# Optimization experiments

Measured on AMD Instinct MI355X. Metric: run time of the kernel, lower is better.

Reference implementation:

```python
import jax, jax.numpy as jnp
import numpy as np

DIM = 1024
HEADS = 16
HEAD_DIM = DIM // HEADS
RANK = 4
AUDIO_DIM = 768


def _lora(x, A, B):
    # x: [..., in]; A: [rank, in]; B: [out, rank]
    return x + (x @ A.T @ B.T) * (1.0 / RANK)


def setup_inputs() -> dict:
    key = jax.random.key(0)
    ks = jax.random.split(key, 20)
    s = 0.02
    inp = {
        "x": jax.random.normal(ks[0], (1, 4096, DIM), jnp.float32),
        "audio_features": jax.random.normal(ks[1], (1, 1024, AUDIO_DIM), jnp.float32),
        "q_w": jax.random.normal(ks[2], (DIM, DIM), jnp.float32) * s,
        "q_b": jnp.zeros((DIM,), jnp.float32),
        "k_w": jax.random.normal(ks[3], (DIM, DIM), jnp.float32) * s,
        "k_b": jnp.zeros((DIM,), jnp.float32),
        "v_w": jax.random.normal(ks[4], (DIM, DIM), jnp.float32) * s,
        "v_b": jnp.zeros((DIM,), jnp.float32),
        "o_w": jax.random.normal(ks[5], (DIM, DIM), jnp.float32) * s,
        "o_b": jnp.zeros((DIM,), jnp.float32),
        "a_w": jax.random.normal(ks[6], (DIM, AUDIO_DIM), jnp.float32) * s,
        "a_b": jnp.zeros((DIM,), jnp.float32),
        "qA": jax.random.normal(ks[7], (RANK, DIM), jnp.float32) * 0.01,
        "qB": jax.random.normal(ks[8], (DIM, RANK), jnp.float32) * 0.01,
        "kA": jax.random.normal(ks[9], (RANK, DIM), jnp.float32) * 0.01,
        "kB": jax.random.normal(ks[10], (DIM, RANK), jnp.float32) * 0.01,
        "vA": jax.random.normal(ks[11], (RANK, DIM), jnp.float32) * 0.01,
        "vB": jax.random.normal(ks[12], (DIM, RANK), jnp.float32) * 0.01,
    }
    return inp


def reference(x, audio_features, q_w, q_b, k_w, k_b, v_w, v_b, o_w, o_b,
              a_w, a_b, qA, qB, kA, kB, vA, vB):
    B, N, C = x.shape
    # audio projection: Linear(768 -> dim), torch Linear is x @ W.T + b
    audio = audio_features @ a_w.T + a_b  # [B, M, C]
    M = audio.shape[1]

    q = _lora(x @ q_w.T + q_b, qA, qB)      # [B, N, C]
    k = _lora(audio @ k_w.T + k_b, kA, kB)  # [B, M, C]
    v = _lora(audio @ v_w.T + v_b, vA, vB)  # [B, M, C]

    q = q.reshape(B, N, HEADS, HEAD_DIM).transpose(0, 2, 1, 3)  # [B,H,N,d]
    k = k.reshape(B, M, HEADS, HEAD_DIM).transpose(0, 2, 1, 3)  # [B,H,M,d]
    v = v.reshape(B, M, HEADS, HEAD_DIM).transpose(0, 2, 1, 3)  # [B,H,M,d]

    scale = HEAD_DIM ** -0.5
    attn = jnp.einsum('bhnd,bhmd->bhnm', q, k) * scale  # [B,H,N,M]
    attn = jax.nn.softmax(attn, axis=-1)
    out = jnp.einsum('bhnm,bhmd->bhnd', attn, v)        # [B,H,N,d]
    out = out.transpose(0, 2, 1, 3).reshape(B, N, C)
    return out @ o_w.T + o_b
```

## Files before the change

### kernel.cpp

```cpp
#include <hip/hip_runtime.h>
#include <math.h>

#define DIM 1024
#define HEADS 16
#define HD 64
#define QSCALE 0.1803368801111204f

typedef __attribute__((ext_vector_type(8))) short short8;
typedef __attribute__((ext_vector_type(4))) float f32x4;
typedef unsigned short ushort_t;

#define MFMA(a, b, c) __builtin_amdgcn_mfma_f32_16x16x32_bf16(a, b, c, 0, 0, 0)
#define VMCNT(n) asm volatile("s_waitcnt vmcnt(" #n ")" ::: "memory")
#define BARRIER() __builtin_amdgcn_s_barrier()

__device__ __forceinline__ ushort_t f2bf(float f) {
    union { float f; unsigned u; } v; v.f = f;
    unsigned r = v.u + 0x7FFF + ((v.u >> 16) & 1);
    return (ushort_t)(r >> 16);
}
__device__ __forceinline__ void gl2lds16(const void* g, void* l) {
    __builtin_amdgcn_global_load_lds(
        (const __attribute__((address_space(1))) unsigned*)g,
        (__attribute__((address_space(3))) unsigned*)l, 16, 0, 0);
}

#define C_X  1048576
#define C_AF 196608
__global__ __launch_bounds__(256) void prep1(
    const float* __restrict__ x, const float* __restrict__ af,
    const float* __restrict__ aw, const float* __restrict__ ow,
    ushort_t* __restrict__ xb, ushort_t* __restrict__ afb,
    ushort_t* __restrict__ awb, ushort_t* __restrict__ owb,
    const float* __restrict__ qw, const float* __restrict__ kw,
    const float* __restrict__ vw,
    const float* __restrict__ qA, const float* __restrict__ kA,
    const float* __restrict__ vA,
    float* __restrict__ part)
{
    const int b = blockIdx.x, tid = threadIdx.x;
    if (b < 6656) {
        int c = b * 256 + tid;
        const float* s; ushort_t* d; int off;
        if (c < C_X)               { s = x;  d = xb;  off = c; }
        else if (c < C_X + C_AF)   { s = af; d = afb; off = c - C_X; }
        else if (c < C_X + 2*C_AF) { s = aw; d = awb; off = c - C_X - C_AF; }
        else                       { s = ow; d = owb; off = c - C_X - 2*C_AF; }
        float4 v = ((const float4*)s)[off];
        ushort4 o = { f2bf(v.x), f2bf(v.y), f2bf(v.z), f2bf(v.w) };
        ((ushort4*)d)[off] = o;
        return;
    }
    const int pb = b - 6656;
    const int proj = pb >> 4, chunk = pb & 15;
    const float* W = proj == 0 ? qw : proj == 1 ? kw : vw;
    const float* A = proj == 0 ? qA : proj == 1 ? kA : vA;
    const float4* W4 = (const float4*)W;

    float4 acc0 = {0,0,0,0}, acc1 = {0,0,0,0}, acc2 = {0,0,0,0}, acc3 = {0,0,0,0};
    const int o0 = chunk * 64;
    for (int o = o0; o < o0 + 64; ++o) {
        float4 wrow = W4[o * 256 + tid];
        float a0 = A[o], a1 = A[1024 + o], a2 = A[2048 + o], a3 = A[3072 + o];
        acc0.x += a0 * wrow.x; acc0.y += a0 * wrow.y; acc0.z += a0 * wrow.z; acc0.w += a0 * wrow.w;
        acc1.x += a1 * wrow.x; acc1.y += a1 * wrow.y; acc1.z += a1 * wrow.z; acc1.w += a1 * wrow.w;
        acc2.x += a2 * wrow.x; acc2.y += a2 * wrow.y; acc2.z += a2 * wrow.z; acc2.w += a2 * wrow.w;
        acc3.x += a3 * wrow.x; acc3.y += a3 * wrow.y; acc3.z += a3 * wrow.z; acc3.w += a3 * wrow.w;
    }
    float4* P4 = (float4*)part;
    P4[(pb * 4 + 0) * 256 + tid] = acc0;
    P4[(pb * 4 + 1) * 256 + tid] = acc1;
    P4[(pb * 4 + 2) * 256 + tid] = acc2;
    P4[(pb * 4 + 3) * 256 + tid] = acc3;
}

__global__ __launch_bounds__(256) void prep2(
    const float* __restrict__ qw, const float* __restrict__ kw,
    const float* __restrict__ vw,
    const float* __restrict__ qA, const float* __restrict__ kA,
    const float* __restrict__ vA,
    const float* __restrict__ qB, const float* __restrict__ kB,
    const float* __restrict__ vB,
    const float* __restrict__ qb, const float* __restrict__ kb,
    const float* __restrict__ vb,
    const float* __restrict__ part,
    ushort_t* __restrict__ wqe, ushort_t* __restrict__ wke,
    ushort_t* __restrict__ wve, float* __restrict__ beff)
{
    const int b = blockIdx.x, tid = threadIdx.x;
    const int proj = b >> 4, chunk = b & 15;
    const float* W = proj == 0 ? qw : proj == 1 ? kw : vw;
    const float* A = proj == 0 ? qA : proj == 1 ? kA : vA;
    const float* B = proj == 0 ? qB : proj == 1 ? kB : vB;
    const float* bias = proj == 0 ? qb : proj == 1 ? kb : vb;
    ushort_t* Weff = proj == 0 ? wqe : proj == 1 ? wke : wve;
    const float scale = proj == 0 ? QSCALE : 1.0f;
    const float4* W4 = (const float4*)W;
    const float4* P4 = (const float4*)part;

    __shared__ float T1s[4096];
    #pragma unroll
    for (int r = 0; r < 4; ++r) {
        float4 s = {0, 0, 0, 0};
        for (int blk = 0; blk < 16; ++blk) {
            float4 p = P4[((proj * 16 + blk) * 4 + r) * 256 + tid];
            s.x += p.x; s.y += p.y; s.z += p.z; s.w += p.w;
        }
        *(float4*)(T1s + r * 1024 + tid * 4) = s;
    }
    __syncthreads();

    float4 t0 = *(const float4*)(T1s + tid * 4);
    float4 t1 = *(const float4*)(T1s + 1024 + tid * 4);
    float4 t2 = *(const float4*)(T1s + 2048 + tid * 4);
    float4 t3 = *(const float4*)(T1s + 3072 + tid * 4);

    const int o0 = chunk * 64;
    for (int o = o0; o < o0 + 64; ++o) {
        float4 wrow = W4[o * 256 + tid];
        float4 Bo = *(const float4*)(B + o * 4);
        ushort4 out;
        out.x = f2bf((wrow.x + 0.25f * (Bo.x*t0.x + Bo.y*t1.x + Bo.z*t2.x + Bo.w*t3.x)) * scale);
        out.y = f2bf((wrow.y + 0.25f * (Bo.x*t0.y + Bo.y*t1.y + Bo.z*t2.y + Bo.w*t3.y)) * scale);
        out.z = f2bf((wrow.z + 0.25f * (Bo.x*t0.z + Bo.y*t1.z + Bo.z*t2.z + Bo.w*t3.z)) * scale);
        out.w = f2bf((wrow.w + 0.25f * (Bo.x*t0.w + Bo.y*t1.w + Bo.z*t2.w + Bo.w*t3.w)) * scale);
        *(ushort4*)(Weff + (size_t)o * 1024 + tid * 4) = out;
    }

    if (chunk == 0) {
        float bt[4] = {0.f, 0.f, 0.f, 0.f};
        for (int o = tid; o < 1024; o += 256) {
            float bo = bias[o];
            bt[0] = fmaf(A[o], bo, bt[0]);
            bt[1] = fmaf(A[1024 + o], bo, bt[1]);
            bt[2] = fmaf(A[2048 + o], bo, bt[2]);
            bt[3] = fmaf(A[3072 + o], bo, bt[3]);
        }
        #pragma unroll
        for (int r = 0; r < 4; ++r)
            #pragma unroll
            for (int off = 32; off; off >>= 1) bt[r] += __shfl_xor(bt[r], off);
        __shared__ float btr[4][4];
        if ((tid & 63) == 0) {
            #pragma unroll
            for (int r = 0; r < 4; ++r) btr[r][tid >> 6] = bt[r];
        }
        __syncthreads();
        float b0 = btr[0][0] + btr[0][1] + btr[0][2] + btr[0][3];
        float b1 = btr[1][0] + btr[1][1] + btr[1][2] + btr[1][3];
        float b2 = btr[2][0] + btr[2][1] + btr[2][2] + btr[2][3];
        float b3 = btr[3][0] + btr[3][1] + btr[3][2] + btr[3][3];
        for (int o = tid; o < 1024; o += 256) {
            float4 Bo = *(const float4*)(B + o * 4);
            beff[proj * 1024 + o] =
                (bias[o] + 0.25f * (Bo.x*b0 + Bo.y*b1 + Bo.z*b2 + Bo.w*b3)) * scale;
        }
    }
}

template<int OUTF32>
__device__ __forceinline__ void gemm3p_body(
    char* lds, const ushort_t* __restrict__ A, const ushort_t* __restrict__ W,
    const float* __restrict__ bias, void* __restrict__ C,
    int N, int K, int bm, int bn)
{
    const int tid = threadIdx.x, lane = tid & 63, wv = tid >> 6;
    const int l15 = lane & 15, l4 = lane >> 4;
    const int wm = wv >> 1, wn = wv & 1;

    const ushort_t *Ag[2], *Wg[2];
    #pragma unroll
    for (int c = 0; c < 2; ++c) {
        int f = c * 256 + tid, ra = f >> 2, ga = (f & 3) ^ ((ra >> 1) & 3);
        Ag[c] = A + (size_t)(bm * 128 + ra) * K + ga * 8;
        Wg[c] = W + (size_t)(bn * 128 + ra) * K + ga * 8;
    }
    int aoff[4], woff[4];
    #pragma unroll
    for (int m = 0; m < 4; ++m) {
        int r = wm * 64 + m * 16 + l15;
        aoff[m] = r * 64 + ((l4 ^ ((r >> 1) & 3)) << 4);
    }
    #pragma unroll
    for (int n = 0; n < 4; ++n) {
        int cc = wn * 64 + n * 16 + l15;
        woff[n] = cc * 64 + ((l4 ^ ((cc >> 1) & 3)) << 4);
    }

    auto stage = [&](char* base, int k0) {
        #pragma unroll
        for (int c = 0; c < 2; ++c) {
            gl2lds16(Ag[c] + k0, base + c * 4096 + wv * 1024);
            gl2lds16(Wg[c] + k0, base + 8192 + c * 4096 + wv * 1024);
        }
    };

    short8 fa[4], fw[4];
    auto readfr = [&](const char* base) {
        #pragma unroll
        for (int m = 0; m < 4; ++m) fa[m] = *(const short8*)(base + aoff[m]);
        #pragma unroll
        for (int n = 0; n < 4; ++n) fw[n] = *(const short8*)(base + 8192 + woff[n]);
    };

    f32x4 acc[4][4] = {};
    const int nt = K / 32;

    stage(lds, 0);
    stage(lds + 16384, 32);
    VMCNT(4);
    BARRIER();
    readfr(lds);

    int bcur = 0;
    for (int t = 0; t < nt; ++t) {
        int bnext = bcur + 1; if (bnext == 3) bnext = 0;
        int bpre  = bnext + 1; if (bpre == 3) bpre = 0;
        if (t + 2 < nt) stage(lds + bpre * 16384, (t + 2) * 32);
        #pragma unroll
        for (int m = 0; m < 4; ++m)
            #pragma unroll
            for (int n = 0; n < 4; ++n)
                acc[m][n] = MFMA(fa[m], fw[n], acc[m][n]);
        if (t + 1 < nt) {
            if (t + 2 < nt) { VMCNT(4); } else { VMCNT(0); }
            BARRIER();
            readfr(lds + bnext * 16384);
        }
        bcur = bnext;
    }

    #pragma unroll
    for (int n = 0; n < 4; ++n) {
        int gc = bn * 128 + wn * 64 + n * 16 + l15;
        float bv = bias[gc];
        #pragma unroll
        for (int m = 0; m < 4; ++m) {
            int gr = bm * 128 + wm * 64 + m * 16 + (l4 << 2);
            #pragma unroll
            for (int j = 0; j < 4; ++j) {
                float v = acc[m][n][j] + bv;
                if (OUTF32) ((float*)C)[(size_t)(gr + j) * N + gc] = v;
                else        ((ushort_t*)C)[(size_t)(gr + j) * N + gc] = f2bf(v);
            }
        }
    }
}

template<int OUTF32>
__global__ __launch_bounds__(256) void gemm3p(
    const ushort_t* __restrict__ A, const ushort_t* __restrict__ W,
    const float* __restrict__ bias, void* __restrict__ C, int N, int K)
{
    __shared__ char lds[49152];
    gemm3p_body<OUTF32>(lds, A, W, bias, C, N, K, blockIdx.y, blockIdx.x);
}

__device__ __forceinline__ void audio_body(
    char* lds, const ushort_t* __restrict__ A, const ushort_t* __restrict__ W,
    const float* __restrict__ bias, ushort_t* __restrict__ C, int bm, int bn)
{
    const int K = 768, N = DIM;
    char* As = lds;
    char* Ws = lds + 8192;
    const int tid = threadIdx.x, lane = tid & 63, wv = tid >> 6;
    const int l15 = lane & 15, l4 = lane >> 4;

    int f = tid, ra = f >> 2, ga = (f & 3) ^ ((ra >> 1) & 3);
    const ushort_t* Ag = A + (size_t)(bm * 64 + ra) * K + ga * 8;
    const ushort_t* Wg = W + (size_t)(bn * 64 + ra) * K + ga * 8;

    int aoff, woff[4];
    { int r = wv * 16 + l15; aoff = r * 64 + ((l4 ^ ((r >> 1) & 3)) << 4); }
    #pragma unroll
    for (int n = 0; n < 4; ++n) {
        int cc = n * 16 + l15;
        woff[n] = cc * 64 + ((l4 ^ ((cc >> 1) & 3)) << 4);
    }

    f32x4 acc[4] = {};
    const int nt = K / 32;
    gl2lds16(Ag, As + wv * 1024);
    gl2lds16(Wg, Ws + wv * 1024);

    for (int t = 0; t < nt; ++t) {
        const int buf = t & 1;
        if (t + 1 < nt) {
            const int k1 = (t + 1) * 32;
            gl2lds16(Ag + k1, As + (buf ^ 1) * 4096 + wv * 1024);
            gl2lds16(Wg + k1, Ws + (buf ^ 1) * 4096 + wv * 1024);
            VMCNT(2);
        } else {
            VMCNT(0);
        }
        BARRIER();
        const char* AsB = As + buf * 4096;
        const char* WsB = Ws + buf * 4096;
        short8 fa = *(const short8*)(AsB + aoff);
        short8 fw[4];
        #pragma unroll
        for (int n = 0; n < 4; ++n) fw[n] = *(const short8*)(WsB + woff[n]);
        #pragma unroll
        for (int n = 0; n < 4; ++n) acc[n] = MFMA(fa, fw[n], acc[n]);
        BARRIER();
    }

    const int gr = bm * 64 + wv * 16 + (l4 << 2);
    #pragma unroll
    for (int n = 0; n < 4; ++n) {
        int gc = bn * 64 + n * 16 + l15;
        float bb = bias[gc];
        #pragma unroll
        for (int j = 0; j < 4; ++j)
            C[(size_t)(gr + j) * N + gc] = f2bf(acc[n][j] + bb);
    }
}

__global__ __launch_bounds__(256) void fused_aq(
    const ushort_t* __restrict__ afb, const ushort_t* __restrict__ awb,
    const float* __restrict__ a_b, ushort_t* __restrict__ audio,
    const ushort_t* __restrict__ xb, const ushort_t* __restrict__ wqe,
    const float* __restrict__ beff, ushort_t* __restrict__ qbb)
{
    __shared__ char lds[49152];
    const int b = blockIdx.x;
    if (b < 256) {
        audio_body(lds, afb, awb, a_b, audio, b >> 4, b & 15);
    } else {
        const int i = b - 256;
        gemm3p_body<0>(lds, xb, wqe, beff, qbb, DIM, DIM, i >> 3, i & 7);
    }
}

__global__ __launch_bounds__(256) void gemm2_kv(
    const ushort_t* __restrict__ A, const ushort_t* __restrict__ Wk,
    const ushort_t* __restrict__ Wv, const float* __restrict__ bk,
    const float* __restrict__ bv, ushort_t* __restrict__ Ck,
    ushort_t* __restrict__ CvT)
{
    const int K = DIM;
    __shared__ ushort_t As[2][64 * 32];
    __shared__ ushort_t Ws[2][64 * 32];
    const int tid = threadIdx.x, lane = tid & 63, wv = tid >> 6;
    const int l15 = lane & 15, l4 = lane >> 4;
    const int bm = blockIdx.y;
    const bool isV = blockIdx.x >= 16;
    const int bn = blockIdx.x & 15;
    const ushort_t* W = isV ? Wv : Wk;

    int f = tid, ra = f >> 2, ga = (f & 3) ^ ((ra >> 1) & 3);
    const ushort_t* Ag = A + (size_t)(bm * 64 + ra) * K + ga * 8;
    const ushort_t* Wg = W + (size_t)(bn * 64 + ra) * K + ga * 8;

    int aoff, woff[4];
    { int r = wv * 16 + l15; aoff = r * 64 + ((l4 ^ ((r >> 1) & 3)) << 4); }
    #pragma unroll
    for (int n = 0; n < 4; ++n) {
        int cc = n * 16 + l15;
        woff[n] = cc * 64 + ((l4 ^ ((cc >> 1) & 3)) << 4);
    }

    f32x4 acc[4] = {};
    const int nt = K / 32;
    gl2lds16(Ag, (char*)As + wv * 1024);
    gl2lds16(Wg, (char*)Ws + wv * 1024);

    for (int t = 0; t < nt; ++t) {
        const int buf = t & 1;
        if (t + 1 < nt) {
            const int k1 = (t + 1) * 32;
            gl2lds16(Ag + k1, (char*)As + (buf ^ 1) * 4096 + wv * 1024);
            gl2lds16(Wg + k1, (char*)Ws + (buf ^ 1) * 4096 + wv * 1024);
            VMCNT(2);
        } else {
            VMCNT(0);
        }
        BARRIER();
        const char* AsB = (const char*)As + buf * 4096;
        const char* WsB = (const char*)Ws + buf * 4096;
        short8 fa = *(const short8*)(AsB + aoff);
        short8 fw[4];
        #pragma unroll
        for (int n = 0; n < 4; ++n) fw[n] = *(const short8*)(WsB + woff[n]);
        #pragma unroll
        for (int n = 0; n < 4; ++n) acc[n] = MFMA(fa, fw[n], acc[n]);
        BARRIER();
    }

    const int gr = bm * 64 + wv * 16 + (l4 << 2);
    #pragma unroll
    for (int n = 0; n < 4; ++n) {
        int gc = bn * 64 + n * 16 + l15;
        float bb = (isV ? bv : bk)[gc];
        if (!isV) {
            #pragma unroll
            for (int j = 0; j < 4; ++j)
                Ck[(size_t)(gr + j) * DIM + gc] = f2bf(acc[n][j] + bb);
        } else {
            ushort4 o = { f2bf(acc[n][0] + bb), f2bf(acc[n][1] + bb),
                          f2bf(acc[n][2] + bb), f2bf(acc[n][3] + bb) };
            *(ushort4*)(CvT + (size_t)gc * DIM + gr) = o;
        }
    }
}

__global__ __launch_bounds__(256) void attn3(
    const ushort_t* __restrict__ Qf, const ushort_t* __restrict__ Kf,
    const ushort_t* __restrict__ Vt, ushort_t* __restrict__ AO)
{
    __shared__ char lds[40960];
    char* QsPs = lds;
    char* KsB0 = lds + 8192;
    char* VsB0 = lds + 24576;

    const int tid = threadIdx.x, lane = tid & 63, wv = tid >> 6;
    const int l15 = lane & 15, l4 = lane >> 4;
    const int h = blockIdx.y, qb = blockIdx.x;

    #pragma unroll
    for (int i = 0; i < 2; ++i) {
        int f = i * 256 + tid, q = f >> 3, s = (f & 7) ^ (q & 7);
        gl2lds16(Qf + (size_t)(qb * 64 + q) * DIM + h * HD + s * 8,
                 QsPs + i * 4096 + wv * 1024);
    }
    const int f0 = tid, r0 = f0 >> 3, s0 = (f0 & 7) ^ (r0 & 7);
    const int f1 = 256 + tid, r1 = f1 >> 3, s1 = (f1 & 7) ^ (r1 & 7);
    const ushort_t* Kg0 = Kf + (size_t)r0 * DIM + h * HD + s0 * 8;
    const ushort_t* Kg1 = Kf + (size_t)r1 * DIM + h * HD + s1 * 8;
    const ushort_t* Vg0 = Vt + (size_t)(h * HD + r0) * DIM + s0 * 8;
    const ushort_t* Vg1 = Vt + (size_t)(h * HD + r1) * DIM + s1 * 8;

    int qoff[2], koff[4][2], poff[2];
    #pragma unroll
    for (int ks = 0; ks < 2; ++ks) {
        int r = wv * 16 + l15;
        qoff[ks] = r * 128 + (((ks * 4 + l4) ^ (r & 7)) << 4);
        poff[ks] = wv * 2048 + l15 * 128 + (((ks * 4 + l4) ^ (l15 & 7)) << 4);
    }
    #pragma unroll
    for (int n = 0; n < 4; ++n) {
        int kk = n * 16 + l15;
        #pragma unroll
        for (int ks = 0; ks < 2; ++ks)
            koff[n][ks] = kk * 128 + (((ks * 4 + l4) ^ (kk & 7)) << 4);
    }

    f32x4 acc_o[4] = {};
    float l_loc[4] = {0.f, 0.f, 0.f, 0.f};

    gl2lds16(Kg0, KsB0 + wv * 1024);
    gl2lds16(Kg1, KsB0 + 4096 + wv * 1024);
    gl2lds16(Vg0, VsB0 + wv * 1024);
    gl2lds16(Vg1, VsB0 + 4096 + wv * 1024);
    VMCNT(4);
    BARRIER();
    short8 fq[2];
    #pragma unroll
    for (int ks = 0; ks < 2; ++ks)
        fq[ks] = *(const short8*)(QsPs + qoff[ks]);

    for (int t = 0; t < 16; ++t) {
        const int buf = t & 1;
        if (t < 15) {
            gl2lds16(Kg0 + (size_t)(t + 1) * 64 * DIM,
                     KsB0 + (buf ^ 1) * 8192 + wv * 1024);
            gl2lds16(Kg1 + (size_t)(t + 1) * 64 * DIM,
                     KsB0 + (buf ^ 1) * 8192 + 4096 + wv * 1024);
            gl2lds16(Vg0 + (t + 1) * 64,
                     VsB0 + (buf ^ 1) * 8192 + wv * 1024);
            gl2lds16(Vg1 + (t + 1) * 64,
                     VsB0 + (buf ^ 1) * 8192 + 4096 + wv * 1024);
            VMCNT(4);
        } else {
            VMCNT(0);
        }
        BARRIER();

        const char* KsT = KsB0 + buf * 8192;
        const char* VsT = VsB0 + buf * 8192;

        f32x4 s_acc[4] = {};
        short8 fk[4][2];
        #pragma unroll
        for (int n = 0; n < 4; ++n)
            #pragma unroll
            for (int ks = 0; ks < 2; ++ks)
                fk[n][ks] = *(const short8*)(KsT + koff[n][ks]);
        #pragma unroll
        for (int n = 0; n < 4; ++n)
            #pragma unroll
            for (int ks = 0; ks < 2; ++ks)
                s_acc[n] = MFMA(fq[ks], fk[n][ks], s_acc[n]);

        #pragma unroll
        for (int j = 0; j < 4; ++j) {
            float p0 = exp2f(s_acc[0][j]);
            float p1 = exp2f(s_acc[1][j]);
            float p2 = exp2f(s_acc[2][j]);
            float p3 = exp2f(s_acc[3][j]);
            l_loc[j] += (p0 + p1) + (p2 + p3);
            unsigned pk01, pk23;
            asm("v_cvt_pk_bf16_f32 %0, %1, %2" : "=v"(pk01) : "v"(p0), "v"(p1));
            asm("v_cvt_pk_bf16_f32 %0, %1, %2" : "=v"(pk23) : "v"(p2), "v"(p3));
            int r16 = (l4 << 2) + j;
            int basb = wv * 2048 + r16 * 128;
            int sw = (r16 & 7) << 4;
            int kx = l15 * 2;
            *(ushort_t*)(QsPs + basb + ((kx) ^ sw))      = (ushort_t)pk01;
            *(ushort_t*)(QsPs + basb + ((32 + kx) ^ sw)) = (ushort_t)(pk01 >> 16);
            *(ushort_t*)(QsPs + basb + ((64 + kx) ^ sw)) = (ushort_t)pk23;
            *(ushort_t*)(QsPs + basb + ((96 + kx) ^ sw)) = (ushort_t)(pk23 >> 16);
        }

        short8 pa[2], fv[4][2];
        #pragma unroll
        for (int ks = 0; ks < 2; ++ks)
            pa[ks] = *(const short8*)(QsPs + poff[ks]);
        #pragma unroll
        for (int n = 0; n < 4; ++n)
            #pragma unroll
            for (int ks = 0; ks < 2; ++ks)
                fv[n][ks] = *(const short8*)(VsT + koff[n][ks]);
        #pragma unroll
        for (int dn = 0; dn < 4; ++dn)
            #pragma unroll
            for (int ks = 0; ks < 2; ++ks)
                acc_o[dn] = MFMA(pa[ks], fv[dn][ks], acc_o[dn]);
        BARRIER();
    }

    #pragma unroll
    for (int j = 0; j < 4; ++j) {
        float l = l_loc[j];
        l += __shfl_xor(l, 1);
        l += __shfl_xor(l, 2);
        l += __shfl_xor(l, 4);
        l += __shfl_xor(l, 8);
        float inv = 1.0f / l;
        int q = qb * 64 + wv * 16 + (l4 << 2) + j;
        #pragma unroll
        for (int dn = 0; dn < 4; ++dn)
            AO[(size_t)q * DIM + h * HD + dn * 16 + l15] =
                f2bf(acc_o[dn][j] * inv);
    }
}

extern "C" void kernel_launch(void* const* d_in, const int* in_sizes, int n_in,
                              void* d_out, int out_size, void* d_ws, size_t ws_size,
                              hipStream_t stream)
{
    const float* x   = (const float*)d_in[0];
    const float* af  = (const float*)d_in[1];
    const float* q_w = (const float*)d_in[2];
    const float* q_b = (const float*)d_in[3];
    const float* k_w = (const float*)d_in[4];
    const float* k_b = (const float*)d_in[5];
    const float* v_w = (const float*)d_in[6];
    const float* v_b = (const float*)d_in[7];
    const float* o_w = (const float*)d_in[8];
    const float* o_b = (const float*)d_in[9];
    const float* a_w = (const float*)d_in[10];
    const float* a_b = (const float*)d_in[11];
    const float* qA  = (const float*)d_in[12];
    const float* qB  = (const float*)d_in[13];
    const float* kA  = (const float*)d_in[14];
    const float* kB  = (const float*)d_in[15];
    const float* vA  = (const float*)d_in[16];
    const float* vB  = (const float*)d_in[17];
    float* out = (float*)d_out;

    const int N = 4096;

    char* w = (char*)d_ws;
    auto alloc = [&](size_t bytes) {
        char* p = w; w += (bytes + 255) & ~(size_t)255; return p;
    };
    ushort_t* xb   = (ushort_t*)alloc((size_t)N * DIM * 2);
    ushort_t* afb  = (ushort_t*)alloc((size_t)1024 * 768 * 2);
    ushort_t* awb  = (ushort_t*)alloc((size_t)DIM * 768 * 2);
    ushort_t* owb  = (ushort_t*)alloc((size_t)DIM * DIM * 2);
    ushort_t* wqe  = (ushort_t*)alloc((size_t)DIM * DIM * 2);
    ushort_t* wke  = (ushort_t*)alloc((size_t)DIM * DIM * 2);
    ushort_t* wve  = (ushort_t*)alloc((size_t)DIM * DIM * 2);
    ushort_t* audio= (ushort_t*)alloc((size_t)1024 * DIM * 2);
    ushort_t* qbb  = (ushort_t*)alloc((size_t)N * DIM * 2);
    ushort_t* kbb  = (ushort_t*)alloc((size_t)1024 * DIM * 2);
    ushort_t* vt   = (ushort_t*)alloc((size_t)1024 * DIM * 2);
    ushort_t* ao   = (ushort_t*)alloc((size_t)N * DIM * 2);
    float* part = (float*)alloc((size_t)48 * 4 * 1024 * 4);
    float* beff = (float*)alloc((size_t)3 * 1024 * 4);

    prep1<<<6704, 256, 0, stream>>>(
        x, af, a_w, o_w, xb, afb, awb, owb,
        q_w, k_w, v_w, qA, kA, vA, part);
    prep2<<<48, 256, 0, stream>>>(
        q_w, k_w, v_w, qA, kA, vA, qB, kB, vB, q_b, k_b, v_b,
        part, wqe, wke, wve, beff);
    fused_aq<<<512, 256, 0, stream>>>(afb, awb, a_b, audio, xb, wqe, beff, qbb);
    gemm2_kv<<<dim3(32, 16), 256, 0, stream>>>(audio, wke, wve,
                                               beff + 1024, beff + 2048, kbb, vt);
    attn3<<<dim3(N / 64, HEADS), 256, 0, stream>>>(qbb, kbb, vt, ao);
    gemm3p<1><<<dim3(8, 32), 256, 0, stream>>>(ao, owb, o_b, out, DIM, DIM);
}
```

Baseline: 230.6 us.

## Split attention keys across two waves with per-wave pipelines and LDS reduction

The attention kernel now runs two waves per block. Each wave owns all 64 queries, holds Q in registers, and processes half of the 1024 keys with its own double-buffered K/V staging, so no block barriers are needed inside the loop. The two partial outputs and row sums are combined through LDS at the end. prep1 also reorders its blocks so the 48 low-rank partial-product blocks are scheduled first. This trades higher register pressure (16 accumulator tiles) and an extra reduction step for fewer barriers and more MFMA work per loaded K/V fragment.

```diff
diff --git a/kernel.cpp b/kernel.cpp
--- a/kernel.cpp
+++ b/kernel.cpp
@@ -12,6 +12,7 @@
 
 #define MFMA(a, b, c) __builtin_amdgcn_mfma_f32_16x16x32_bf16(a, b, c, 0, 0, 0)
 #define VMCNT(n) asm volatile("s_waitcnt vmcnt(" #n ")" ::: "memory")
+#define LGKMCNT0() asm volatile("s_waitcnt lgkmcnt(0)" ::: "memory")
 #define BARRIER() __builtin_amdgcn_s_barrier()
 
 __device__ __forceinline__ ushort_t f2bf(float f) {
@@ -39,8 +40,8 @@
     float* __restrict__ part)
 {
     const int b = blockIdx.x, tid = threadIdx.x;
-    if (b < 6656) {
-        int c = b * 256 + tid;
+    if (b >= 48) {
+        int c = (b - 48) * 256 + tid;
         const float* s; ushort_t* d; int off;
         if (c < C_X)               { s = x;  d = xb;  off = c; }
         else if (c < C_X + C_AF)   { s = af; d = afb; off = c - C_X; }
@@ -51,7 +52,7 @@
         ((ushort4*)d)[off] = o;
         return;
     }
-    const int pb = b - 6656;
+    const int pb = b;
     const int proj = pb >> 4, chunk = pb & 15;
     const float* W = proj == 0 ? qw : proj == 1 ? kw : vw;
     const float* A = proj == 0 ? qA : proj == 1 ? kA : vA;
@@ -404,144 +405,158 @@
     }
 }
 
-__global__ __launch_bounds__(256) void attn3(
+__global__ __launch_bounds__(128) void attn4(
     const ushort_t* __restrict__ Qf, const ushort_t* __restrict__ Kf,
     const ushort_t* __restrict__ Vt, ushort_t* __restrict__ AO)
 {
-    __shared__ char lds[40960];
-    char* QsPs = lds;
-    char* KsB0 = lds + 8192;
-    char* VsB0 = lds + 24576;
-
-    const int tid = threadIdx.x, lane = tid & 63, wv = tid >> 6;
+    __shared__ char lds[41472];
+    char* KL = lds;
+    char* VL = lds + 16384;
+    char* PL = lds + 32768;
+    float* l_arr = (float*)(lds + 40960);
+
+    const int tid = threadIdx.x, lane = tid & 63, w = tid >> 6;
     const int l15 = lane & 15, l4 = lane >> 4;
     const int h = blockIdx.y, qb = blockIdx.x;
-
-    #pragma unroll
-    for (int i = 0; i < 2; ++i) {
-        int f = i * 256 + tid, q = f >> 3, s = (f & 7) ^ (q & 7);
-        gl2lds16(Qf + (size_t)(qb * 64 + q) * DIM + h * HD + s * 8,
-                 QsPs + i * 4096 + wv * 1024);
-    }
-    const int f0 = tid, r0 = f0 >> 3, s0 = (f0 & 7) ^ (r0 & 7);
-    const int f1 = 256 + tid, r1 = f1 >> 3, s1 = (f1 & 7) ^ (r1 & 7);
-    const ushort_t* Kg0 = Kf + (size_t)r0 * DIM + h * HD + s0 * 8;
-    const ushort_t* Kg1 = Kf + (size_t)r1 * DIM + h * HD + s1 * 8;
-    const ushort_t* Vg0 = Vt + (size_t)(h * HD + r0) * DIM + s0 * 8;
-    const ushort_t* Vg1 = Vt + (size_t)(h * HD + r1) * DIM + s1 * 8;
-
-    int qoff[2], koff[4][2], poff[2];
-    #pragma unroll
-    for (int ks = 0; ks < 2; ++ks) {
-        int r = wv * 16 + l15;
-        qoff[ks] = r * 128 + (((ks * 4 + l4) ^ (r & 7)) << 4);
-        poff[ks] = wv * 2048 + l15 * 128 + (((ks * 4 + l4) ^ (l15 & 7)) << 4);
-    }
-    #pragma unroll
-    for (int n = 0; n < 4; ++n) {
+    const int key_base = w * 512;
+
+    short8 fq[4][2];
+    #pragma unroll
+    for (int m = 0; m < 4; ++m)
+        #pragma unroll
+        for (int ks = 0; ks < 2; ++ks)
+            fq[m][ks] = *(const short8*)(
+                Qf + (size_t)(qb * 64 + m * 16 + l15) * DIM + h * HD + (ks * 4 + l4) * 8);
+
+    char* Kw = KL + w * 8192;
+    char* Vw = VL + w * 8192;
+    char* Pw = PL + w * 4096;
+
+    auto stageK = [&](int t, int buf) {
+        int k0 = key_base + t * 32;
+        #pragma unroll
+        for (int i = 0; i < 4; ++i) {
+            int f = i * 64 + lane, row = f >> 3, s = (f & 7) ^ (row & 7);
+            gl2lds16(Kf + (size_t)(k0 + row) * DIM + h * HD + s * 8,
+                     Kw + buf * 4096 + i * 1024);
+        }
+    };
+    auto stageV = [&](int t, int buf) {
+        int k0 = key_base + t * 32;
+        #pragma unroll
+        for (int i = 0; i < 4; ++i) {
+            int f = i * 64 + lane, row = f >> 2, s = (f & 3) ^ ((row >> 1) & 3);
+            gl2lds16(Vt + (size_t)(h * HD + row) * DIM + k0 + s * 8,
+                     Vw + buf * 4096 + i * 1024);
+        }
+    };
+
+    int koff[2][2], voff[4], poffR[4];
+    #pragma unroll
+    for (int n = 0; n < 2; ++n) {
         int kk = n * 16 + l15;
         #pragma unroll
         for (int ks = 0; ks < 2; ++ks)
             koff[n][ks] = kk * 128 + (((ks * 4 + l4) ^ (kk & 7)) << 4);
     }
-
-    f32x4 acc_o[4] = {};
-    float l_loc[4] = {0.f, 0.f, 0.f, 0.f};
-
-    gl2lds16(Kg0, KsB0 + wv * 1024);
-    gl2lds16(Kg1, KsB0 + 4096 + wv * 1024);
-    gl2lds16(Vg0, VsB0 + wv * 1024);
-    gl2lds16(Vg1, VsB0 + 4096 + wv * 1024);
-    VMCNT(4);
-    BARRIER();
-    short8 fq[2];
-    #pragma unroll
-    for (int ks = 0; ks < 2; ++ks)
-        fq[ks] = *(const short8*)(QsPs + qoff[ks]);
+    #pragma unroll
+    for (int dn = 0; dn < 4; ++dn) {
+        int d = dn * 16 + l15;
+        voff[dn] = d * 64 + ((l4 ^ ((d >> 1) & 3)) << 4);
+    }
+    #pragma unroll
+    for (int m = 0; m < 4; ++m) {
+        int r = m * 16 + l15;
+        poffR[m] = r * 64 + ((l4 ^ ((r >> 1) & 3)) << 4);
+    }
+
+    f32x4 acc_o[4][4] = {};
+    float l_loc[4][4] = {};
+
+    stageK(0, 0); stageV(0, 0);
+    stageK(1, 1); stageV(1, 1);
 
     for (int t = 0; t < 16; ++t) {
         const int buf = t & 1;
-        if (t < 15) {
-            gl2lds16(Kg0 + (size_t)(t + 1) * 64 * DIM,
-                     KsB0 + (buf ^ 1) * 8192 + wv * 1024);
-            gl2lds16(Kg1 + (size_t)(t + 1) * 64 * DIM,
-                     KsB0 + (buf ^ 1) * 8192 + 4096 + wv * 1024);
-            gl2lds16(Vg0 + (t + 1) * 64,
-                     VsB0 + (buf ^ 1) * 8192 + wv * 1024);
-            gl2lds16(Vg1 + (t + 1) * 64,
-                     VsB0 + (buf ^ 1) * 8192 + 4096 + wv * 1024);
-            VMCNT(4);
-        } else {
-            VMCNT(0);
-        }
-        BARRIER();
-
-        const char* KsT = KsB0 + buf * 8192;
-        const char* VsT = VsB0 + buf * 8192;
-
-        f32x4 s_acc[4] = {};
-        short8 fk[4][2];
-        #pragma unroll
-        for (int n = 0; n < 4; ++n)
+        if (t < 15) { VMCNT(8); } else { VMCNT(0); }
+        const char* Kb = Kw + buf * 4096;
+        const char* Vb = Vw + buf * 4096;
+
+        short8 fk[2][2];
+        #pragma unroll
+        for (int n = 0; n < 2; ++n)
             #pragma unroll
             for (int ks = 0; ks < 2; ++ks)
-                fk[n][ks] = *(const short8*)(KsT + koff[n][ks]);
-        #pragma unroll
-        for (int n = 0; n < 4; ++n)
-            #pragma unroll
-            for (int ks = 0; ks < 2; ++ks)
-                s_acc[n] = MFMA(fq[ks], fk[n][ks], s_acc[n]);
-
+                fk[n][ks] = *(const short8*)(Kb + koff[n][ks]);
+
+        #pragma unroll
+        for (int m = 0; m < 4; ++m) {
+            f32x4 s0 = {}, s1 = {};
+            s0 = MFMA(fq[m][0], fk[0][0], s0);
+            s0 = MFMA(fq[m][1], fk[0][1], s0);
+            s1 = MFMA(fq[m][0], fk[1][0], s1);
+            s1 = MFMA(fq[m][1], fk[1][1], s1);
+            #pragma unroll
+            for (int j = 0; j < 4; ++j) {
+                float p0 = exp2f(s0[j]);
+                float p1 = exp2f(s1[j]);
+                l_loc[m][j] += p0 + p1;
+                int row = m * 16 + (l4 << 2) + j;
+                int swz = (row >> 1) & 3;
+                int b0 = row * 64 + ((((l15 >> 3)) ^ swz) << 4) + (l15 & 7) * 2;
+                int b1 = row * 64 + ((((16 + l15) >> 3) ^ swz) << 4) + (l15 & 7) * 2;
+                *(ushort_t*)(Pw + b0) = f2bf(p0);
+                *(ushort_t*)(Pw + b1) = f2bf(p1);
+            }
+        }
+
+        LGKMCNT0();
+        short8 fv[4];
+        #pragma unroll
+        for (int dn = 0; dn < 4; ++dn)
+            fv[dn] = *(const short8*)(Vb + voff[dn]);
+        #pragma unroll
+        for (int m = 0; m < 4; ++m) {
+            short8 pa = *(const short8*)(Pw + poffR[m]);
+            #pragma unroll
+            for (int dn = 0; dn < 4; ++dn)
+                acc_o[m][dn] = MFMA(pa, fv[dn], acc_o[m][dn]);
+        }
+
+        if (t + 2 < 16) {
+            LGKMCNT0();
+            __builtin_amdgcn_sched_barrier(0);
+            stageK(t + 2, buf); stageV(t + 2, buf);
+        }
+    }
+
+    #pragma unroll
+    for (int m = 0; m < 4; ++m)
         #pragma unroll
         for (int j = 0; j < 4; ++j) {
-            float p0 = exp2f(s_acc[0][j]);
-            float p1 = exp2f(s_acc[1][j]);
-            float p2 = exp2f(s_acc[2][j]);
-            float p3 = exp2f(s_acc[3][j]);
-            l_loc[j] += (p0 + p1) + (p2 + p3);
-            unsigned pk01, pk23;
-            asm("v_cvt_pk_bf16_f32 %0, %1, %2" : "=v"(pk01) : "v"(p0), "v"(p1));
-            asm("v_cvt_pk_bf16_f32 %0, %1, %2" : "=v"(pk23) : "v"(p2), "v"(p3));
-            int r16 = (l4 << 2) + j;
-            int basb = wv * 2048 + r16 * 128;
-            int sw = (r16 & 7) << 4;
-            int kx = l15 * 2;
-            *(ushort_t*)(QsPs + basb + ((kx) ^ sw))      = (ushort_t)pk01;
-            *(ushort_t*)(QsPs + basb + ((32 + kx) ^ sw)) = (ushort_t)(pk01 >> 16);
-            *(ushort_t*)(QsPs + basb + ((64 + kx) ^ sw)) = (ushort_t)pk23;
-            *(ushort_t*)(QsPs + basb + ((96 + kx) ^ sw)) = (ushort_t)(pk23 >> 16);
-        }
-
-        short8 pa[2], fv[4][2];
-        #pragma unroll
-        for (int ks = 0; ks < 2; ++ks)
-            pa[ks] = *(const short8*)(QsPs + poff[ks]);
-        #pragma unroll
-        for (int n = 0; n < 4; ++n)
-            #pragma unroll
-            for (int ks = 0; ks < 2; ++ks)
-                fv[n][ks] = *(const short8*)(VsT + koff[n][ks]);
+            float l = l_loc[m][j];
+            l += __shfl_xor(l, 1);
+            l += __shfl_xor(l, 2);
+            l += __shfl_xor(l, 4);
+            l += __shfl_xor(l, 8);
+            if (l15 == 0) l_arr[w * 64 + m * 16 + (l4 << 2) + j] = l;
+        }
+    __syncthreads();
+    float* OP = (float*)lds;
+    #pragma unroll
+    for (int m = 0; m < 4; ++m)
         #pragma unroll
         for (int dn = 0; dn < 4; ++dn)
             #pragma unroll
-            for (int ks = 0; ks < 2; ++ks)
-                acc_o[dn] = MFMA(pa[ks], fv[dn][ks], acc_o[dn]);
-        BARRIER();
-    }
-
-    #pragma unroll
-    for (int j = 0; j < 4; ++j) {
-        float l = l_loc[j];
-        l += __shfl_xor(l, 1);
-        l += __shfl_xor(l, 2);
-        l += __shfl_xor(l, 4);
-        l += __shfl_xor(l, 8);
-        float inv = 1.0f / l;
-        int q = qb * 64 + wv * 16 + (l4 << 2) + j;
-        #pragma unroll
-        for (int dn = 0; dn < 4; ++dn)
-            AO[(size_t)q * DIM + h * HD + dn * 16 + l15] =
-                f2bf(acc_o[dn][j] * inv);
+            for (int j = 0; j < 4; ++j)
+                OP[w * 4096 + (m * 16 + (l4 << 2) + j) * 64 + dn * 16 + l15] =
+                    acc_o[m][dn][j];
+    __syncthreads();
+    for (int rr = 0; rr < 32; ++rr) {
+        int row = w * 32 + rr;
+        float o = OP[row * 64 + lane] + OP[4096 + row * 64 + lane];
+        float lt = l_arr[row] + l_arr[64 + row];
+        AO[(size_t)(qb * 64 + row) * DIM + h * HD + lane] = f2bf(o / lt);
     }
 }
 
@@ -599,6 +614,6 @@
     fused_aq<<<512, 256, 0, stream>>>(afb, awb, a_b, audio, xb, wqe, beff, qbb);
     gemm2_kv<<<dim3(32, 16), 256, 0, stream>>>(audio, wke, wve,
                                                beff + 1024, beff + 2048, kbb, vt);
-    attn3<<<dim3(N / 64, HEADS), 256, 0, stream>>>(qbb, kbb, vt, ao);
+    attn4<<<dim3(N / 64, HEADS), 128, 0, stream>>>(qbb, kbb, vt, ao);
     gemm3p<1><<<dim3(8, 32), 256, 0, stream>>>(ao, owb, o_b, out, DIM, DIM);
 }
```

Result: slower. 250.2 us (+8.5%).
